# Optimization experiments

Measured on AMD Instinct MI355X. Metric: run time of the kernel, lower is better.

## Reference

```python
import jax, jax.numpy as jnp
import numpy as np

IMG = 28      # image side
WS = 2        # window (patch) side
NPS = IMG // WS          # patches per side = 14
NP = NPS * NPS           # 196 patches
NW = 12                  # circuit weights: 4+2+4+2
NC = 10                  # classes
B = 512                  # batch

_CX = jnp.array([[1, 0, 0, 0],
                 [0, 1, 0, 0],
                 [0, 0, 0, 1],
                 [0, 0, 1, 0]], dtype=jnp.complex64)  # basis |control,target>


def _ry(theta):
    # RY(theta) = [[cos(t/2), -sin(t/2)], [sin(t/2), cos(t/2)]]; theta scalar or (M,)
    c = jnp.cos(theta * 0.5)
    s = jnp.sin(theta * 0.5)
    return jnp.stack([jnp.stack([c, -s], -1),
                      jnp.stack([s, c], -1)], -2).astype(jnp.complex64)


def _crx(theta):
    # controlled-RX, 4x4 in |control,target> basis (identity on control=0 block)
    c = jnp.cos(theta * 0.5).astype(jnp.complex64)
    s = jnp.sin(theta * 0.5).astype(jnp.complex64)
    U = jnp.eye(4, dtype=jnp.complex64)
    U = U.at[2, 2].set(c).at[3, 3].set(c)
    U = U.at[2, 3].set(-1j * s).at[3, 2].set(-1j * s)
    return U


def _ap1(st, U, q):
    # apply 1-qubit gate U (2,2) or per-sample (M,2,2) on qubit q; st: (M,2,2,2,2)
    st = jnp.moveaxis(st, 1 + q, 4)
    if U.ndim == 2:
        st = jnp.einsum('ij,mabcj->mabci', U, st)
    else:
        st = jnp.einsum('mij,mabcj->mabci', U, st)
    return jnp.moveaxis(st, 4, 1 + q)


def _ap2(st, U, qc, qt):
    # apply 2-qubit gate U (4,4) with control qc, target qt
    st = jnp.moveaxis(st, (1 + qc, 1 + qt), (3, 4))
    M = st.shape[0]
    st = jnp.einsum('ij,mabj->mabi', U, st.reshape(M, 2, 2, 4)).reshape(M, 2, 2, 2, 2)
    return jnp.moveaxis(st, (3, 4), (1 + qc, 1 + qt))


def _qcnn(angles, qw):
    # angles: (M,4) input rotation angles; qw: (12,) shared circuit weights
    # returns (M,3) Bloch vector [<X>,<Y>,<Z>] of qubit 0
    M = angles.shape[0]
    st = jnp.zeros((M, 2, 2, 2, 2), jnp.complex64).at[:, 0, 0, 0, 0].set(1.0)
    for q in range(4):                       # data encoding
        st = _ap1(st, _ry(angles[:, q]), q)
    # conv1
    st = _ap1(st, _ry(qw[0]), 0)
    st = _ap1(st, _ry(qw[1]), 1)
    st = _ap2(st, _CX, 0, 1)
    st = _ap1(st, _ry(qw[2]), 2)
    st = _ap1(st, _ry(qw[3]), 3)
    st = _ap2(st, _CX, 2, 3)
    st = _ap2(st, _CX, 1, 2)
    st = _ap2(st, _CX, 3, 0)
    # pool1
    st = _ap2(st, _crx(qw[4]), 1, 0)
    st = _ap2(st, _crx(qw[5]), 3, 2)
    # conv2
    st = _ap1(st, _ry(qw[6]), 0)
    st = _ap1(st, _ry(qw[7]), 2)
    st = _ap2(st, _CX, 0, 2)
    st = _ap1(st, _ry(qw[8]), 0)
    st = _ap1(st, _ry(qw[9]), 2)
    # pool2
    st = _ap2(st, _crx(qw[10]), 2, 0)
    st = _ap1(st, _ry(qw[11]), 0)
    # expectations on qubit 0 via reduced density matrix entries
    a = jnp.moveaxis(st, 1, 4).reshape(M, 8, 2)       # (M, other-qubits, qubit0)
    r01 = jnp.sum(a[:, :, 0] * jnp.conj(a[:, :, 1]), axis=1)
    ex = 2.0 * jnp.real(r01)
    ey = -2.0 * jnp.imag(r01)
    p0 = jnp.sum(jnp.real(a[:, :, 0] * jnp.conj(a[:, :, 0])), axis=1)
    p1 = jnp.sum(jnp.real(a[:, :, 1] * jnp.conj(a[:, :, 1])), axis=1)
    return jnp.stack([ex, ey, p0 - p1], -1)


def setup_inputs() -> dict:
    key = jax.random.key(0)
    k1, k2, k3 = jax.random.split(key, 3)
    x = jax.random.uniform(k1, (B, 1, IMG, IMG), jnp.float32)         # pixel values in [0,1]
    qw = jax.random.uniform(k2, (NW,), jnp.float32, -1.0, 1.0)         # circuit weights
    fc_w = jax.random.normal(k3, (NC, NP * 3), jnp.float32) * 0.02
    fc_b = jnp.zeros((NC,), jnp.float32)
    return {"x": x, "qw": qw, "fc_w": fc_w, "fc_b": fc_b}


def reference(x, qw, fc_w, fc_b):
    b = x.shape[0]
    img = x.reshape(b, IMG, IMG)
    # 2x2 stride-2 patches, row-major within patch (matches torch unfold+view)
    p = img.reshape(b, NPS, WS, NPS, WS).transpose(0, 1, 3, 2, 4).reshape(b, NP, WS * WS)
    angles = (p * jnp.pi).reshape(b * NP, 4)
    feats = _qcnn(angles, qw).reshape(b, NP * 3)      # (B, 588)
    return feats @ fc_w.T + fc_b                      # (B, 10)
```

## Files before the change

### kernel.cpp

```cpp
#include <hip/hip_runtime.h>
#include <math.h>

#define IMGS 28
#define NPSD 14
#define NPAT 196
#define NCLS 10
#define NFEAT (NPAT * 3)

__device__ __forceinline__ void fsincos(float x, float& s, float& c) {
    s = __sinf(x);
    c = __cosf(x);
}


template <int MASK>
__device__ __forceinline__ void ry_gate(float (&sr)[16], float (&si)[16], float c, float s) {
#pragma unroll
    for (int i = 0; i < 16; ++i) {
        if (i & MASK) continue;
        const int j = i | MASK;
        float r0 = sr[i], q0 = si[i], r1 = sr[j], q1 = si[j];
        sr[i] = c * r0 - s * r1;  si[i] = c * q0 - s * q1;
        sr[j] = s * r0 + c * r1;  si[j] = s * q0 + c * q1;
    }
}

template <int MC, int MT>
__device__ __forceinline__ void cx_gate(float (&sr)[16], float (&si)[16]) {
#pragma unroll
    for (int i = 0; i < 16; ++i) {
        if ((i & MC) && !(i & MT)) {
            const int j = i | MT;
            float tr = sr[i], ti = si[i];
            sr[i] = sr[j]; si[i] = si[j];
            sr[j] = tr;    si[j] = ti;
        }
    }
}

template <int MC, int MT>
__device__ __forceinline__ void crx_gate(float (&sr)[16], float (&si)[16], float c, float s) {
#pragma unroll
    for (int i = 0; i < 16; ++i) {
        if ((i & MC) && !(i & MT)) {
            const int j = i | MT;
            float r0 = sr[i], q0 = si[i], r1 = sr[j], q1 = si[j];
            sr[i] = c * r0 + s * q1;  si[i] = c * q0 - s * r1;
            sr[j] = c * r1 + s * q0;  si[j] = c * q1 - s * r0;
        }
    }
}

__global__ __launch_bounds__(256) void qcnn_fused_kernel(
        const float* __restrict__ x, const float* __restrict__ qw,
        const float* __restrict__ fc_w, const float* __restrict__ fc_b,
        float* __restrict__ out) {
    __shared__ float partial[4][NCLS];

    const int b = blockIdx.x;
    const int t = threadIdx.x;

    float con[NCLS];
#pragma unroll
    for (int c = 0; c < NCLS; ++c) con[c] = 0.0f;

    if (t < NPAT) {
        const int pr = t / NPSD, pc = t % NPSD;
        const float* img = x + (size_t)b * (IMGS * IMGS);
        const float* p0 = img + (2 * pr) * IMGS + 2 * pc;
        const float a0 = p0[0], a1 = p0[1], a2 = p0[IMGS], a3 = p0[IMGS + 1];

        float ce[4], se[4];
        const float HPI = 1.57079632679489662f;
        fsincos(a0 * HPI, se[0], ce[0]);
        fsincos(a1 * HPI, se[1], ce[1]);
        fsincos(a2 * HPI, se[2], ce[2]);
        fsincos(a3 * HPI, se[3], ce[3]);

        float sr[16], si[16];
#pragma unroll
        for (int i = 0; i < 16; ++i) {
            float v = ((i & 8) ? se[0] : ce[0]) * ((i & 4) ? se[1] : ce[1]) *
                      ((i & 2) ? se[2] : ce[2]) * ((i & 1) ? se[3] : ce[3]);
            sr[i] = v;
            si[i] = 0.0f;
        }

        float cw[12], sw[12];
#pragma unroll
        for (int i = 0; i < 12; ++i) fsincos(qw[i] * 0.5f, sw[i], cw[i]);

        ry_gate<8>(sr, si, cw[0], sw[0]);
        ry_gate<4>(sr, si, cw[1], sw[1]);
        cx_gate<8, 4>(sr, si);
        ry_gate<2>(sr, si, cw[2], sw[2]);
        ry_gate<1>(sr, si, cw[3], sw[3]);
        cx_gate<2, 1>(sr, si);
        cx_gate<4, 2>(sr, si);
        cx_gate<1, 8>(sr, si);
        crx_gate<4, 8>(sr, si, cw[4], sw[4]);
        crx_gate<1, 2>(sr, si, cw[5], sw[5]);
        ry_gate<8>(sr, si, cw[6], sw[6]);
        ry_gate<2>(sr, si, cw[7], sw[7]);
        cx_gate<8, 2>(sr, si);
        ry_gate<8>(sr, si, cw[8], sw[8]);
        ry_gate<2>(sr, si, cw[9], sw[9]);
        crx_gate<2, 8>(sr, si, cw[10], sw[10]);
        ry_gate<8>(sr, si, cw[11], sw[11]);

        float ex = 0.f, ey = 0.f, ez = 0.f;
#pragma unroll
        for (int j = 0; j < 8; ++j) {
            float r0 = sr[j], q0 = si[j], r1 = sr[j + 8], q1 = si[j + 8];
            ex += r0 * r1 + q0 * q1;
            ey += r0 * q1 - q0 * r1;
            ez += (r0 * r0 + q0 * q0) - (r1 * r1 + q1 * q1);
        }
        ex *= 2.0f;
        ey *= 2.0f;

#pragma unroll
        for (int c = 0; c < NCLS; ++c) {
            const float* w = fc_w + c * NFEAT + 3 * t;
            con[c] = ex * w[0] + ey * w[1] + ez * w[2];
        }
    }

#pragma unroll
    for (int c = 0; c < NCLS; ++c) {
        float v = con[c];
#pragma unroll
        for (int off = 32; off >= 1; off >>= 1) v += __shfl_xor(v, off, 64);
        con[c] = v;
    }

    const int wave = t >> 6, lane = t & 63;
    if (lane == 0) {
#pragma unroll
        for (int c = 0; c < NCLS; ++c) partial[wave][c] = con[c];
    }
    __syncthreads();

    if (t < NCLS) {
        out[b * NCLS + t] = partial[0][t] + partial[1][t] + partial[2][t] +
                            partial[3][t] + fc_b[t];
    }
}

extern "C" void kernel_launch(void* const* d_in, const int* in_sizes, int n_in,
                              void* d_out, int out_size, void* d_ws, size_t ws_size,
                              hipStream_t stream) {
    const float* x    = (const float*)d_in[0];
    const float* qw   = (const float*)d_in[1];
    const float* fc_w = (const float*)d_in[2];
    const float* fc_b = (const float*)d_in[3];
    float* out = (float*)d_out;

    const int B = in_sizes[0] / (IMGS * IMGS);
    qcnn_fused_kernel<<<B, 256, 0, stream>>>(x, qw, fc_w, fc_b, out);
}
```

Measured before the change: 10.16 us.

## Split each patch's 16-amplitude state across two lanes with shuffle-based gates

Each patch's 4-qubit statevector is now split across a lane pair, with the qubit-3 index mapped to the lane bit. Each thread holds 8 amplitudes, and gates on the split qubit use __shfl_xor exchanges and lane-dependent selects. Blocks grow to 512 threads and image loads use float2. The aim is to halve per-thread registers and serial work, at the cost of extra cross-lane shuffles, doubled FC-weight reads and a larger reduction.

```diff
diff --git a/kernel.cpp b/kernel.cpp
--- a/kernel.cpp
+++ b/kernel.cpp
@@ -14,104 +14,153 @@
 
 
 template <int MASK>
-__device__ __forceinline__ void ry_gate(float (&sr)[16], float (&si)[16], float c, float s) {
-#pragma unroll
-    for (int i = 0; i < 16; ++i) {
-        if (i & MASK) continue;
-        const int j = i | MASK;
-        float r0 = sr[i], q0 = si[i], r1 = sr[j], q1 = si[j];
-        sr[i] = c * r0 - s * r1;  si[i] = c * q0 - s * q1;
-        sr[j] = s * r0 + c * r1;  si[j] = s * q0 + c * q1;
+__device__ __forceinline__ void ry8r(float (&hr)[8], float c, float s) {
+#pragma unroll
+    for (int k = 0; k < 8; ++k) {
+        if (k & MASK) continue;
+        const int j = k | MASK;
+        float r0 = hr[k], r1 = hr[j];
+        hr[k] = c * r0 - s * r1;
+        hr[j] = s * r0 + c * r1;
+    }
+}
+
+template <int MASK>
+__device__ __forceinline__ void ry8(float (&hr)[8], float (&hi)[8], float c, float s) {
+#pragma unroll
+    for (int k = 0; k < 8; ++k) {
+        if (k & MASK) continue;
+        const int j = k | MASK;
+        float r0 = hr[k], q0 = hi[k], r1 = hr[j], q1 = hi[j];
+        hr[k] = c * r0 - s * r1;  hi[k] = c * q0 - s * q1;
+        hr[j] = s * r0 + c * r1;  hi[j] = s * q0 + c * q1;
     }
 }
 
 template <int MC, int MT>
-__device__ __forceinline__ void cx_gate(float (&sr)[16], float (&si)[16]) {
-#pragma unroll
-    for (int i = 0; i < 16; ++i) {
-        if ((i & MC) && !(i & MT)) {
-            const int j = i | MT;
-            float tr = sr[i], ti = si[i];
-            sr[i] = sr[j]; si[i] = si[j];
-            sr[j] = tr;    si[j] = ti;
-        }
-    }
+__device__ __forceinline__ void cx8r(float (&hr)[8]) {
+#pragma unroll
+    for (int k = 0; k < 8; ++k)
+        if ((k & MC) && !(k & MT)) {
+            const int j = k | MT;
+            float t = hr[k]; hr[k] = hr[j]; hr[j] = t;
+        }
 }
 
 template <int MC, int MT>
-__device__ __forceinline__ void crx_gate(float (&sr)[16], float (&si)[16], float c, float s) {
-#pragma unroll
-    for (int i = 0; i < 16; ++i) {
-        if ((i & MC) && !(i & MT)) {
-            const int j = i | MT;
-            float r0 = sr[i], q0 = si[i], r1 = sr[j], q1 = si[j];
-            sr[i] = c * r0 + s * q1;  si[i] = c * q0 - s * r1;
-            sr[j] = c * r1 + s * q0;  si[j] = c * q1 - s * r0;
-        }
-    }
-}
-
-__global__ __launch_bounds__(256) void qcnn_fused_kernel(
+__device__ __forceinline__ void cx8(float (&hr)[8], float (&hi)[8]) {
+#pragma unroll
+    for (int k = 0; k < 8; ++k)
+        if ((k & MC) && !(k & MT)) {
+            const int j = k | MT;
+            float t = hr[k]; hr[k] = hr[j]; hr[j] = t;
+            t = hi[k]; hi[k] = hi[j]; hi[j] = t;
+        }
+}
+
+template <int MC, int MT>
+__device__ __forceinline__ void crx8(float (&hr)[8], float (&hi)[8], float c, float s) {
+#pragma unroll
+    for (int k = 0; k < 8; ++k) {
+        if ((k & MC) && !(k & MT)) {
+            const int j = k | MT;
+            float r0 = hr[k], q0 = hi[k], r1 = hr[j], q1 = hi[j];
+            hr[k] = c * r0 + s * q1;  hi[k] = c * q0 - s * r1;
+            hr[j] = c * r1 + s * q0;  hi[j] = c * q1 - s * r0;
+        }
+    }
+}
+
+__global__ __launch_bounds__(512) void qcnn_split_kernel(
         const float* __restrict__ x, const float* __restrict__ qw,
         const float* __restrict__ fc_w, const float* __restrict__ fc_b,
         float* __restrict__ out) {
-    __shared__ float partial[4][NCLS];
+    __shared__ float partial[8][NCLS];
 
     const int b = blockIdx.x;
     const int t = threadIdx.x;
+    const int p = t >> 1;
+    const int e = t & 1;
 
     float con[NCLS];
 #pragma unroll
     for (int c = 0; c < NCLS; ++c) con[c] = 0.0f;
 
-    if (t < NPAT) {
-        const int pr = t / NPSD, pc = t % NPSD;
+    if (p < NPAT) {
+        const int pr = p / NPSD, pc = p % NPSD;
         const float* img = x + (size_t)b * (IMGS * IMGS);
-        const float* p0 = img + (2 * pr) * IMGS + 2 * pc;
-        const float a0 = p0[0], a1 = p0[1], a2 = p0[IMGS], a3 = p0[IMGS + 1];
-
-        float ce[4], se[4];
+        const float2 rw0 = *(const float2*)(img + (2 * pr) * IMGS + 2 * pc);
+        const float2 rw1 = *(const float2*)(img + (2 * pr + 1) * IMGS + 2 * pc);
+
         const float HPI = 1.57079632679489662f;
-        fsincos(a0 * HPI, se[0], ce[0]);
-        fsincos(a1 * HPI, se[1], ce[1]);
-        fsincos(a2 * HPI, se[2], ce[2]);
-        fsincos(a3 * HPI, se[3], ce[3]);
-
-        float sr[16], si[16];
-#pragma unroll
-        for (int i = 0; i < 16; ++i) {
-            float v = ((i & 8) ? se[0] : ce[0]) * ((i & 4) ? se[1] : ce[1]) *
-                      ((i & 2) ? se[2] : ce[2]) * ((i & 1) ? se[3] : ce[3]);
-            sr[i] = v;
-            si[i] = 0.0f;
+        float c0, s0, c1, s1, c2, s2, c3, s3;
+        fsincos(rw0.x * HPI, s0, c0);
+        fsincos(rw0.y * HPI, s1, c1);
+        fsincos(rw1.x * HPI, s2, c2);
+        fsincos(rw1.y * HPI, s3, c3);
+        const float t3 = e ? s3 : c3;
+
+        float hr[8], hi[8];
+#pragma unroll
+        for (int k = 0; k < 8; ++k) {
+            hr[k] = ((k & 4) ? s0 : c0) * ((k & 2) ? s1 : c1) * ((k & 1) ? s2 : c2) * t3;
+            hi[k] = 0.0f;
         }
 
         float cw[12], sw[12];
 #pragma unroll
         for (int i = 0; i < 12; ++i) fsincos(qw[i] * 0.5f, sw[i], cw[i]);
 
-        ry_gate<8>(sr, si, cw[0], sw[0]);
-        ry_gate<4>(sr, si, cw[1], sw[1]);
-        cx_gate<8, 4>(sr, si);
-        ry_gate<2>(sr, si, cw[2], sw[2]);
-        ry_gate<1>(sr, si, cw[3], sw[3]);
-        cx_gate<2, 1>(sr, si);
-        cx_gate<4, 2>(sr, si);
-        cx_gate<1, 8>(sr, si);
-        crx_gate<4, 8>(sr, si, cw[4], sw[4]);
-        crx_gate<1, 2>(sr, si, cw[5], sw[5]);
-        ry_gate<8>(sr, si, cw[6], sw[6]);
-        ry_gate<2>(sr, si, cw[7], sw[7]);
-        cx_gate<8, 2>(sr, si);
-        ry_gate<8>(sr, si, cw[8], sw[8]);
-        ry_gate<2>(sr, si, cw[9], sw[9]);
-        crx_gate<2, 8>(sr, si, cw[10], sw[10]);
-        ry_gate<8>(sr, si, cw[11], sw[11]);
+        ry8r<4>(hr, cw[0], sw[0]);
+        ry8r<2>(hr, cw[1], sw[1]);
+        cx8r<4, 2>(hr);
+        ry8r<1>(hr, cw[2], sw[2]);
+        {
+            const float ssel = e ? sw[3] : -sw[3];
+#pragma unroll
+            for (int k = 0; k < 8; ++k) {
+                float pv = __shfl_xor(hr[k], 1, 64);
+                hr[k] = cw[3] * hr[k] + ssel * pv;
+            }
+        }
+#pragma unroll
+        for (int k = 1; k < 8; k += 2) hr[k] = __shfl_xor(hr[k], 1, 64);
+        cx8r<2, 1>(hr);
+        {
+            float old[8];
+#pragma unroll
+            for (int k = 0; k < 8; ++k) old[k] = hr[k];
+#pragma unroll
+            for (int k = 0; k < 8; ++k) hr[k] = e ? old[k ^ 4] : old[k];
+        }
+
+        crx8<2, 4>(hr, hi, cw[4], sw[4]);
+        {
+            const float cc = e ? cw[5] : 1.0f;
+            const float ss = e ? sw[5] : 0.0f;
+#pragma unroll
+            for (int k = 0; k < 8; k += 2) {
+                const int j = k | 1;
+                float ra = hr[k], qa = hi[k], rb = hr[j], qb = hi[j];
+                hr[k] = cc * ra + ss * qb;  hi[k] = cc * qa - ss * rb;
+                hr[j] = cc * rb + ss * qa;  hi[j] = cc * qb - ss * ra;
+            }
+        }
+
+        ry8<4>(hr, hi, cw[6], sw[6]);
+        ry8<1>(hr, hi, cw[7], sw[7]);
+        cx8<4, 1>(hr, hi);
+        ry8<4>(hr, hi, cw[8], sw[8]);
+        ry8<1>(hr, hi, cw[9], sw[9]);
+
+        crx8<1, 4>(hr, hi, cw[10], sw[10]);
+        ry8<4>(hr, hi, cw[11], sw[11]);
 
         float ex = 0.f, ey = 0.f, ez = 0.f;
 #pragma unroll
-        for (int j = 0; j < 8; ++j) {
-            float r0 = sr[j], q0 = si[j], r1 = sr[j + 8], q1 = si[j + 8];
+        for (int k = 0; k < 4; ++k) {
+            const int j = k | 4;
+            float r0 = hr[k], q0 = hi[k], r1 = hr[j], q1 = hi[j];
             ex += r0 * r1 + q0 * q1;
             ey += r0 * q1 - q0 * r1;
             ez += (r0 * r0 + q0 * q0) - (r1 * r1 + q1 * q1);
@@ -121,7 +170,7 @@
 
 #pragma unroll
         for (int c = 0; c < NCLS; ++c) {
-            const float* w = fc_w + c * NFEAT + 3 * t;
+            const float* w = fc_w + c * NFEAT + 3 * p;
             con[c] = ex * w[0] + ey * w[1] + ez * w[2];
         }
     }
@@ -142,8 +191,10 @@
     __syncthreads();
 
     if (t < NCLS) {
-        out[b * NCLS + t] = partial[0][t] + partial[1][t] + partial[2][t] +
-                            partial[3][t] + fc_b[t];
+        float acc = fc_b[t];
+#pragma unroll
+        for (int w = 0; w < 8; ++w) acc += partial[w][t];
+        out[b * NCLS + t] = acc;
     }
 }
 
@@ -157,5 +208,5 @@
     float* out = (float*)d_out;
 
     const int B = in_sizes[0] / (IMGS * IMGS);
-    qcnn_fused_kernel<<<B, 256, 0, stream>>>(x, qw, fc_w, fc_b, out);
-}
+    qcnn_split_kernel<<<B, 512, 0, stream>>>(x, qw, fc_w, fc_b, out);
+}
```

Result: slower. 18.00 us (+77.1%).
